# Performance work log

Measured on AMD Instinct MI355X. Metric: run time of the kernel, lower is better.

## Reference

```python
import jax, jax.numpy as jnp
from jax import lax
import numpy as np

S, B, I, H, O = 65536, 1, 2, 128, 1


def setup_inputs() -> dict:
    key = jax.random.key(0)
    k1, k2, k3, k4 = jax.random.split(key, 4)
    # xavier_normal-style scales
    s_ih = (2.0 / (4 * H + I)) ** 0.5
    s_hh = (2.0 / (4 * H + H)) ** 0.5
    s_out = (2.0 / (H + O)) ** 0.5
    return {
        "x": jax.random.normal(k1, (S, B, I), jnp.float32),
        "h0": jnp.zeros((1, B, H), jnp.float32),
        "c0": jnp.zeros((1, B, H), jnp.float32),
        "W_ih": jax.random.normal(k2, (4 * H, I), jnp.float32) * s_ih,
        "W_hh": jax.random.normal(k3, (4 * H, H), jnp.float32) * s_hh,
        "b_ih": jnp.zeros((4 * H,), jnp.float32),
        "b_hh": jnp.zeros((4 * H,), jnp.float32),
        "W_out": jax.random.normal(k4, (O, H), jnp.float32) * s_out,
        "b_out": jnp.zeros((O,), jnp.float32),
    }


def reference(x, h0, c0, W_ih, W_hh, b_ih, b_hh, W_out, b_out):
    # Precompute input-to-gate projections for all timesteps: (S, B, 4H)
    xg = jnp.einsum("sbi,gi->sbg", x, W_ih) + b_ih + b_hh

    def step(carry, xg_t):
        h, c = carry  # (B, H) each
        gates = xg_t + h @ W_hh.T  # (B, 4H); PyTorch order i,f,g,o
        i, f, g, o = jnp.split(gates, 4, axis=-1)
        i = jax.nn.sigmoid(i)
        f = jax.nn.sigmoid(f)
        g = jnp.tanh(g)
        o = jax.nn.sigmoid(o)
        c = f * c + i * g
        h = o * jnp.tanh(c)
        return (h, c), h

    (_, _), hs = lax.scan(step, (h0[0], c0[0]), xg)  # hs: (S, B, H)
    out = jnp.tanh(hs.transpose(1, 0, 2))  # (B, S, H), matches permute(1,0,2)
    out = out @ W_out.T + b_out  # (B, S, O)
    return out.reshape(out.shape[0] * out.shape[1], -1)  # (B*S, O)
```

## Files before the change

kernel.cpp:

```cpp
#include <hip/hip_runtime.h>

#define S_LEN 65536
#define HDIM 128

typedef _Float16 half2_t __attribute__((ext_vector_type(2)));
typedef _Float16 half8_t __attribute__((ext_vector_type(8)));
typedef float f32x4 __attribute__((ext_vector_type(4)));

__device__ __forceinline__ float sigm(float x) {
    return 1.0f / (1.0f + __expf(-x));
}
__device__ __forceinline__ float tanh_fast(float x) {
    return 2.0f / (1.0f + __expf(-2.0f * x)) - 1.0f;
}
__device__ __forceinline__ float dot2(half2_t a, half2_t b, float c) {
#if __has_builtin(__builtin_amdgcn_fdot2)
    return __builtin_amdgcn_fdot2(a, b, c, false);
#else
    return fmaf((float)a.x, (float)b.x, fmaf((float)a.y, (float)b.y, c));
#endif
}

__global__ __launch_bounds__(512)
__attribute__((amdgpu_waves_per_eu(2, 2)))
void lstm_seq_mfma(const float* __restrict__ x,
                   const float* __restrict__ h0,
                   const float* __restrict__ c0,
                   const float* __restrict__ W_ih,
                   const float* __restrict__ W_hh,
                   const float* __restrict__ b_ih,
                   const float* __restrict__ b_hh,
                   _Float16* __restrict__ h_hist)
{
    __shared__ __align__(16) _Float16 h_sh16[HDIM];
    __shared__ __align__(16) float gates_sh[4 * HDIM];

    const int tid  = threadIdx.x;
    const int lane = tid & 63;
    const int w    = tid >> 6;
    const int m    = lane & 15;
    const int quad = lane >> 4;

#define LOAD_AF(i, q) \
    half8_t af_##i##_##q; { \
        const float* s_ = W_hh + (size_t)(w * 64 + 16 * (i) + m) * HDIM \
                               + 32 * (q) + 8 * quad; \
        af_##i##_##q = (half8_t){ \
            (_Float16)s_[0], (_Float16)s_[1], (_Float16)s_[2], (_Float16)s_[3], \
            (_Float16)s_[4], (_Float16)s_[5], (_Float16)s_[6], (_Float16)s_[7] }; \
        asm volatile("" : "+v"(af_##i##_##q)); }
    LOAD_AF(0, 0) LOAD_AF(0, 1) LOAD_AF(0, 2) LOAD_AF(0, 3)
    LOAD_AF(1, 0) LOAD_AF(1, 1) LOAD_AF(1, 2) LOAD_AF(1, 3)
    LOAD_AF(2, 0) LOAD_AF(2, 1) LOAD_AF(2, 2) LOAD_AF(2, 3)
    LOAD_AF(3, 0) LOAD_AF(3, 1) LOAD_AF(3, 2) LOAD_AF(3, 3)
#undef LOAD_AF

    float wi0x = 0.f, wi0y = 0.f, bs0 = 0.f;
    float wi1x = 0.f, wi1y = 0.f, bs1 = 0.f;
    float wi2x = 0.f, wi2y = 0.f, bs2 = 0.f;
    float wi3x = 0.f, wi3y = 0.f, bs3 = 0.f;
    float c = 0.0f;
    if (tid < HDIM) {
        wi0x = W_ih[2 * tid];            wi0y = W_ih[2 * tid + 1];
        wi1x = W_ih[2 * (tid + 128)];    wi1y = W_ih[2 * (tid + 128) + 1];
        wi2x = W_ih[2 * (tid + 256)];    wi2y = W_ih[2 * (tid + 256) + 1];
        wi3x = W_ih[2 * (tid + 384)];    wi3y = W_ih[2 * (tid + 384) + 1];
        bs0 = b_ih[tid]       + b_hh[tid];
        bs1 = b_ih[tid + 128] + b_hh[tid + 128];
        bs2 = b_ih[tid + 256] + b_hh[tid + 256];
        bs3 = b_ih[tid + 384] + b_hh[tid + 384];
        c = c0[tid];
        h_sh16[tid] = (_Float16)h0[tid];
    }
    __syncthreads();

    const float2* xp = (const float2*)x;
    float2 xcur = {0.f, 0.f}, xnext = {0.f, 0.f};
    if (tid < HDIM) xcur = xp[0];

    half8_t bf0 = (half8_t){0,0,0,0,0,0,0,0};
    half8_t bf1 = bf0, bf2 = bf0, bf3 = bf0;

    #pragma unroll 1
    for (int t = 0; t < S_LEN; ++t) {
        if (m == 0) {
            const half8_t* hb = (const half8_t*)h_sh16;
            bf0 = hb[quad];
            bf1 = hb[4 + quad];
            bf2 = hb[8 + quad];
            bf3 = hb[12 + quad];
        }
        f32x4 acc0 = {0.f, 0.f, 0.f, 0.f};
        f32x4 acc1 = {0.f, 0.f, 0.f, 0.f};
        f32x4 acc2 = {0.f, 0.f, 0.f, 0.f};
        f32x4 acc3 = {0.f, 0.f, 0.f, 0.f};
#define MFMA_TILE(i) \
        acc##i = __builtin_amdgcn_mfma_f32_16x16x32_f16(af_##i##_0, bf0, acc##i, 0, 0, 0); \
        acc##i = __builtin_amdgcn_mfma_f32_16x16x32_f16(af_##i##_1, bf1, acc##i, 0, 0, 0); \
        acc##i = __builtin_amdgcn_mfma_f32_16x16x32_f16(af_##i##_2, bf2, acc##i, 0, 0, 0); \
        acc##i = __builtin_amdgcn_mfma_f32_16x16x32_f16(af_##i##_3, bf3, acc##i, 0, 0, 0);
        MFMA_TILE(0) MFMA_TILE(1) MFMA_TILE(2) MFMA_TILE(3)
#undef MFMA_TILE
        if (m == 0) {
            f32x4* gp = (f32x4*)gates_sh + w * 16 + quad;
            gp[0]  = acc0;
            gp[4]  = acc1;
            gp[8]  = acc2;
            gp[12] = acc3;
        }

        if (tid < HDIM) {
            const int tn = (t + 1 < S_LEN) ? (t + 1) : (S_LEN - 1);
            xnext = xp[tn];
        }
        __syncthreads();

        if (tid < HDIM) {
            float gi = sigm(gates_sh[tid]
                            + fmaf(wi0x, xcur.x, fmaf(wi0y, xcur.y, bs0)));
            float gf = sigm(gates_sh[tid + 128]
                            + fmaf(wi1x, xcur.x, fmaf(wi1y, xcur.y, bs1)));
            float gg = tanh_fast(gates_sh[tid + 256]
                            + fmaf(wi2x, xcur.x, fmaf(wi2y, xcur.y, bs2)));
            float go = sigm(gates_sh[tid + 384]
                            + fmaf(wi3x, xcur.x, fmaf(wi3y, xcur.y, bs3)));
            c = fmaf(gf, c, gi * gg);
            float h = go * tanh_fast(c);
            _Float16 hf = (_Float16)h;
            h_sh16[tid] = hf;
            h_hist[t * HDIM + tid] = hf;
            xcur = xnext;
        }
        __syncthreads();
    }
}

__global__ __launch_bounds__(256)
void out_proj(const _Float16* __restrict__ h_hist,
              const float* __restrict__ W_out,
              const float* __restrict__ b_out,
              float* __restrict__ out)
{
    const int lane  = threadIdx.x & 63;
    const int gwave = (blockIdx.x * 256 + threadIdx.x) >> 6;
    const int nwave = (gridDim.x * 256) >> 6;

    const float wo0 = W_out[2 * lane + 0];
    const float wo1 = W_out[2 * lane + 1];
    const float bout = b_out[0];

    for (int t = gwave; t < S_LEN; t += nwave) {
        half2_t hv = ((const half2_t*)(h_hist + t * HDIM))[lane];
        float p = tanh_fast((float)hv.x) * wo0 + tanh_fast((float)hv.y) * wo1;
        #pragma unroll
        for (int off = 32; off > 0; off >>= 1)
            p += __shfl_xor(p, off, 64);
        if (lane == 0) out[t] = p + bout;
    }
}

#define H_HI_OFF 144
__global__ __launch_bounds__(1024)
__attribute__((amdgpu_waves_per_eu(4, 4)))
void lstm_seq_full(const float* __restrict__ x,
                   const float* __restrict__ h0,
                   const float* __restrict__ c0,
                   const float* __restrict__ W_ih,
                   const float* __restrict__ W_hh,
                   const float* __restrict__ b_ih,
                   const float* __restrict__ b_hh,
                   const float* __restrict__ W_out,
                   const float* __restrict__ b_out,
                   float* __restrict__ out)
{
    __shared__ __align__(16) unsigned char h_raw[2 * H_HI_OFF];
    __shared__ float gates_part[2 * 512];
    __shared__ float red_sh[2];

    const int tid  = threadIdx.x;
    const int j    = tid >> 1;
    const int half = tid & 1;

    const float2* wr2 = (const float2*)(W_hh + j * HDIM + half * 64);
#define WDEF(i) half2_t W##i; { float2 t = wr2[i]; \
        W##i.x = (_Float16)t.x; W##i.y = (_Float16)t.y; } \
        asm volatile("" : "+v"(W##i));
    WDEF(0)  WDEF(1)  WDEF(2)  WDEF(3)  WDEF(4)  WDEF(5)  WDEF(6)  WDEF(7)
    WDEF(8)  WDEF(9)  WDEF(10) WDEF(11) WDEF(12) WDEF(13) WDEF(14) WDEF(15)
    WDEF(16) WDEF(17) WDEF(18) WDEF(19) WDEF(20) WDEF(21) WDEF(22) WDEF(23)
    WDEF(24) WDEF(25) WDEF(26) WDEF(27) WDEF(28) WDEF(29) WDEF(30) WDEF(31)
#undef WDEF

    float wih0 = 0.0f, wih1 = 0.0f, bias = 0.0f;
    if (half == 0) {
        wih0 = W_ih[2 * j + 0];
        wih1 = W_ih[2 * j + 1];
        bias = b_ih[j] + b_hh[j];
    }

    float c = 0.0f, wout = 0.0f;
    _Float16* hw = (_Float16*)(h_raw + ((tid < 64) ? 2 * tid
                                                   : H_HI_OFF + 2 * (tid - 64)));
    if (tid < HDIM) {
        c = c0[tid];
        wout = W_out[tid];
        *hw = (_Float16)h0[tid];
    }
    const float bout = b_out[0];
    __syncthreads();

    const float2* xp = (const float2*)x;
    float2 xcur = xp[0];
    const half8_t* hp = (const half8_t*)(h_raw + half * H_HI_OFF);

    #pragma unroll 1
    for (int t = 0; t < S_LEN; ++t) {
        const int tn = (t + 1 < S_LEN) ? (t + 1) : (S_LEN - 1);
        float2 xnext = xp[tn];

        float a0 = fmaf(wih0, xcur.x, fmaf(wih1, xcur.y, bias));
        float a1 = 0.0f, a2 = 0.0f, a3 = 0.0f;

#define CHUNK(cc, w0_, w1_, w2_, w3_) {                         \
        half8_t hv = hp[cc];                                    \
        half2_t p0 = { hv[0], hv[1] };                          \
        half2_t p1 = { hv[2], hv[3] };                          \
        half2_t p2 = { hv[4], hv[5] };                          \
        half2_t p3 = { hv[6], hv[7] };                          \
        a0 = dot2(w0_, p0, a0);                                 \
        a1 = dot2(w1_, p1, a1);                                 \
        a2 = dot2(w2_, p2, a2);                                 \
        a3 = dot2(w3_, p3, a3); }
        CHUNK(0, W0,  W1,  W2,  W3)
        CHUNK(1, W4,  W5,  W6,  W7)
        CHUNK(2, W8,  W9,  W10, W11)
        CHUNK(3, W12, W13, W14, W15)
        CHUNK(4, W16, W17, W18, W19)
        CHUNK(5, W20, W21, W22, W23)
        CHUNK(6, W24, W25, W26, W27)
        CHUNK(7, W28, W29, W30, W31)
#undef CHUNK

        gates_part[half * 512 + j] = (a0 + a1) + (a2 + a3);
        __syncthreads();

        if (tid < HDIM) {
            float gi = sigm(gates_part[tid]            + gates_part[tid + 512]);
            float gf = sigm(gates_part[tid + 128]      + gates_part[tid + 640]);
            float gg = tanh_fast(gates_part[tid + 256] + gates_part[tid + 768]);
            float go = sigm(gates_part[tid + 384]      + gates_part[tid + 896]);
            c = fmaf(gf, c, gi * gg);
            float h = go * tanh_fast(c);
            *hw = (_Float16)h;

            float p = tanh_fast(h) * wout;
            #pragma unroll
            for (int off = 32; off > 0; off >>= 1)
                p += __shfl_xor(p, off, 64);
            if ((tid & 63) == 0) red_sh[tid >> 6] = p;
        }
        __syncthreads();

        if (tid == 0) out[t] = red_sh[0] + red_sh[1] + bout;
        xcur = xnext;
    }
}

extern "C" void kernel_launch(void* const* d_in, const int* in_sizes, int n_in,
                              void* d_out, int out_size, void* d_ws, size_t ws_size,
                              hipStream_t stream) {
    const float* x     = (const float*)d_in[0];
    const float* h0    = (const float*)d_in[1];
    const float* c0    = (const float*)d_in[2];
    const float* W_ih  = (const float*)d_in[3];
    const float* W_hh  = (const float*)d_in[4];
    const float* b_ih  = (const float*)d_in[5];
    const float* b_hh  = (const float*)d_in[6];
    const float* W_out = (const float*)d_in[7];
    const float* b_out = (const float*)d_in[8];

    const size_t need = (size_t)S_LEN * HDIM * sizeof(_Float16);
    if (ws_size >= need) {
        _Float16* h_hist = (_Float16*)d_ws;
        lstm_seq_mfma<<<dim3(1), dim3(512), 0, stream>>>(
            x, h0, c0, W_ih, W_hh, b_ih, b_hh, h_hist);
        out_proj<<<dim3(1024), dim3(256), 0, stream>>>(
            h_hist, W_out, b_out, (float*)d_out);
    } else {
        lstm_seq_full<<<dim3(1), dim3(1024), 0, stream>>>(
            x, h0, c0, W_ih, W_hh, b_ih, b_hh, W_out, b_out, (float*)d_out);
    }
}
```

Baseline: 46.68 ms.

## Compute LSTM gates in MFMA lanes with double-buffered h and single barrier

Reorders W_hh rows so each wave's four MFMA tiles hold the i,f,g,o gates for the same 16 hidden units. Lanes with m<4 now apply the nonlinearities directly from their accumulator registers, which removes the gates_sh round-trip through shared memory. With h double-buffered, each timestep needs one barrier instead of two, and that barrier is a raw s_barrier. x is prefetched two steps ahead and the loop is unrolled by two. In exchange, the pointwise work is spread across all eight waves, and correctness now depends on the MFMA output layout and on the hand-placed waitcnt before the barrier.

```diff
diff --git a/kernel.cpp b/kernel.cpp
--- a/kernel.cpp
+++ b/kernel.cpp
@@ -20,6 +20,12 @@
     return fmaf((float)a.x, (float)b.x, fmaf((float)a.y, (float)b.y, c));
 #endif
 }
+
+#define WG_BARRIER() do {                                         \
+    asm volatile("s_waitcnt lgkmcnt(0)" ::: "memory");            \
+    __builtin_amdgcn_s_barrier();                                 \
+    asm volatile("" ::: "memory");                                \
+} while (0)
 
 __global__ __launch_bounds__(512)
 __attribute__((amdgpu_waves_per_eu(2, 2)))
@@ -32,8 +38,7 @@
                    const float* __restrict__ b_hh,
                    _Float16* __restrict__ h_hist)
 {
-    __shared__ __align__(16) _Float16 h_sh16[HDIM];
-    __shared__ __align__(16) float gates_sh[4 * HDIM];
+    __shared__ __align__(16) _Float16 h_buf[2][HDIM];
 
     const int tid  = threadIdx.x;
     const int lane = tid & 63;
@@ -41,98 +46,100 @@
     const int m    = lane & 15;
     const int quad = lane >> 4;
 
-#define LOAD_AF(i, q) \
-    half8_t af_##i##_##q; { \
-        const float* s_ = W_hh + (size_t)(w * 64 + 16 * (i) + m) * HDIM \
-                               + 32 * (q) + 8 * quad; \
-        af_##i##_##q = (half8_t){ \
+#define LOAD_AF(i, cc) \
+    half8_t af_##i##_##cc; { \
+        const float* s_ = W_hh + (size_t)((i) * 128 + w * 16 + m) * HDIM \
+                               + 32 * (cc) + 8 * quad; \
+        af_##i##_##cc = (half8_t){ \
             (_Float16)s_[0], (_Float16)s_[1], (_Float16)s_[2], (_Float16)s_[3], \
             (_Float16)s_[4], (_Float16)s_[5], (_Float16)s_[6], (_Float16)s_[7] }; \
-        asm volatile("" : "+v"(af_##i##_##q)); }
+        asm volatile("" : "+v"(af_##i##_##cc)); }
     LOAD_AF(0, 0) LOAD_AF(0, 1) LOAD_AF(0, 2) LOAD_AF(0, 3)
     LOAD_AF(1, 0) LOAD_AF(1, 1) LOAD_AF(1, 2) LOAD_AF(1, 3)
     LOAD_AF(2, 0) LOAD_AF(2, 1) LOAD_AF(2, 2) LOAD_AF(2, 3)
     LOAD_AF(3, 0) LOAD_AF(3, 1) LOAD_AF(3, 2) LOAD_AF(3, 3)
 #undef LOAD_AF
 
-    float wi0x = 0.f, wi0y = 0.f, bs0 = 0.f;
-    float wi1x = 0.f, wi1y = 0.f, bs1 = 0.f;
-    float wi2x = 0.f, wi2y = 0.f, bs2 = 0.f;
-    float wi3x = 0.f, wi3y = 0.f, bs3 = 0.f;
+    const bool worker = (m < 4);
+    const int  hidx   = w * 16 + quad * 4 + (m & 3);
+    float wi00 = 0.f, wi01 = 0.f, bs0 = 0.f;
+    float wi10 = 0.f, wi11 = 0.f, bs1 = 0.f;
+    float wi20 = 0.f, wi21 = 0.f, bs2 = 0.f;
+    float wi30 = 0.f, wi31 = 0.f, bs3 = 0.f;
     float c = 0.0f;
-    if (tid < HDIM) {
-        wi0x = W_ih[2 * tid];            wi0y = W_ih[2 * tid + 1];
-        wi1x = W_ih[2 * (tid + 128)];    wi1y = W_ih[2 * (tid + 128) + 1];
-        wi2x = W_ih[2 * (tid + 256)];    wi2y = W_ih[2 * (tid + 256) + 1];
-        wi3x = W_ih[2 * (tid + 384)];    wi3y = W_ih[2 * (tid + 384) + 1];
-        bs0 = b_ih[tid]       + b_hh[tid];
-        bs1 = b_ih[tid + 128] + b_hh[tid + 128];
-        bs2 = b_ih[tid + 256] + b_hh[tid + 256];
-        bs3 = b_ih[tid + 384] + b_hh[tid + 384];
-        c = c0[tid];
-        h_sh16[tid] = (_Float16)h0[tid];
-    }
+    if (worker) {
+        const int r0 = hidx;
+        const int r1 = hidx + 128;
+        const int r2 = hidx + 256;
+        const int r3 = hidx + 384;
+        wi00 = W_ih[2 * r0]; wi01 = W_ih[2 * r0 + 1]; bs0 = b_ih[r0] + b_hh[r0];
+        wi10 = W_ih[2 * r1]; wi11 = W_ih[2 * r1 + 1]; bs1 = b_ih[r1] + b_hh[r1];
+        wi20 = W_ih[2 * r2]; wi21 = W_ih[2 * r2 + 1]; bs2 = b_ih[r2] + b_hh[r2];
+        wi30 = W_ih[2 * r3]; wi31 = W_ih[2 * r3 + 1]; bs3 = b_ih[r3] + b_hh[r3];
+        c = c0[hidx];
+    }
+    if (tid < HDIM) h_buf[0][tid] = (_Float16)h0[tid];
     __syncthreads();
 
     const float2* xp = (const float2*)x;
-    float2 xcur = {0.f, 0.f}, xnext = {0.f, 0.f};
-    if (tid < HDIM) xcur = xp[0];
-
-    half8_t bf0 = (half8_t){0,0,0,0,0,0,0,0};
-    half8_t bf1 = bf0, bf2 = bf0, bf3 = bf0;
+    float2 xcur = xp[0];
+    float2 xn1  = xp[1];
+
+    const bool selod = (m & 1) != 0;
+    const bool selhi = (m & 2) != 0;
+
+#define MFMA_T(i) \
+    acc##i = __builtin_amdgcn_mfma_f32_16x16x32_f16(af_##i##_0, bf0, acc##i, 0, 0, 0); \
+    acc##i = __builtin_amdgcn_mfma_f32_16x16x32_f16(af_##i##_1, bf1, acc##i, 0, 0, 0); \
+    acc##i = __builtin_amdgcn_mfma_f32_16x16x32_f16(af_##i##_2, bf2, acc##i, 0, 0, 0); \
+    acc##i = __builtin_amdgcn_mfma_f32_16x16x32_f16(af_##i##_3, bf3, acc##i, 0, 0, 0);
+
+#define STEP(T, RB, WB) { \
+     \
+    const half8_t* hb_ = (const half8_t*)(RB); \
+    half8_t bf0 = hb_[quad]; \
+    half8_t bf1 = hb_[4 + quad]; \
+    half8_t bf2 = hb_[8 + quad]; \
+    half8_t bf3 = hb_[12 + quad]; \
+    f32x4 acc0 = {0.f, 0.f, 0.f, 0.f}; \
+    f32x4 acc1 = acc0, acc2 = acc0, acc3 = acc0; \
+    MFMA_T(0) MFMA_T(1) MFMA_T(2) MFMA_T(3) \
+    int tn_ = (T) + 2; if (tn_ >= S_LEN) tn_ = S_LEN - 1; \
+    float2 xnew_ = xp[tn_]; \
+    const float xg0 = fmaf(wi00, xcur.x, fmaf(wi01, xcur.y, bs0)); \
+    const float xg1 = fmaf(wi10, xcur.x, fmaf(wi11, xcur.y, bs1)); \
+    const float xg2 = fmaf(wi20, xcur.x, fmaf(wi21, xcur.y, bs2)); \
+    const float xg3 = fmaf(wi30, xcur.x, fmaf(wi31, xcur.y, bs3)); \
+    if (worker) { \
+        float sa_, sb_; \
+        sa_ = selod ? acc0[1] : acc0[0]; sb_ = selod ? acc0[3] : acc0[2]; \
+        const float g0 = (selhi ? sb_ : sa_) + xg0; \
+        sa_ = selod ? acc1[1] : acc1[0]; sb_ = selod ? acc1[3] : acc1[2]; \
+        const float g1 = (selhi ? sb_ : sa_) + xg1; \
+        sa_ = selod ? acc2[1] : acc2[0]; sb_ = selod ? acc2[3] : acc2[2]; \
+        const float g2 = (selhi ? sb_ : sa_) + xg2; \
+        sa_ = selod ? acc3[1] : acc3[0]; sb_ = selod ? acc3[3] : acc3[2]; \
+        const float g3 = (selhi ? sb_ : sa_) + xg3; \
+        const float gi = sigm(g0); \
+        const float gf = sigm(g1); \
+        const float gg = tanh_fast(g2); \
+        const float go = sigm(g3); \
+        c = fmaf(gf, c, gi * gg); \
+        const float hv_ = go * tanh_fast(c); \
+        const _Float16 hf_ = (_Float16)hv_; \
+        (WB)[hidx] = hf_;                        \
+        h_hist[(size_t)(T) * HDIM + hidx] = hf_;  \
+    } \
+    xcur = xn1; xn1 = xnew_; \
+    WG_BARRIER(); }
 
     #pragma unroll 1
-    for (int t = 0; t < S_LEN; ++t) {
-        if (m == 0) {
-            const half8_t* hb = (const half8_t*)h_sh16;
-            bf0 = hb[quad];
-            bf1 = hb[4 + quad];
-            bf2 = hb[8 + quad];
-            bf3 = hb[12 + quad];
-        }
-        f32x4 acc0 = {0.f, 0.f, 0.f, 0.f};
-        f32x4 acc1 = {0.f, 0.f, 0.f, 0.f};
-        f32x4 acc2 = {0.f, 0.f, 0.f, 0.f};
-        f32x4 acc3 = {0.f, 0.f, 0.f, 0.f};
-#define MFMA_TILE(i) \
-        acc##i = __builtin_amdgcn_mfma_f32_16x16x32_f16(af_##i##_0, bf0, acc##i, 0, 0, 0); \
-        acc##i = __builtin_amdgcn_mfma_f32_16x16x32_f16(af_##i##_1, bf1, acc##i, 0, 0, 0); \
-        acc##i = __builtin_amdgcn_mfma_f32_16x16x32_f16(af_##i##_2, bf2, acc##i, 0, 0, 0); \
-        acc##i = __builtin_amdgcn_mfma_f32_16x16x32_f16(af_##i##_3, bf3, acc##i, 0, 0, 0);
-        MFMA_TILE(0) MFMA_TILE(1) MFMA_TILE(2) MFMA_TILE(3)
-#undef MFMA_TILE
-        if (m == 0) {
-            f32x4* gp = (f32x4*)gates_sh + w * 16 + quad;
-            gp[0]  = acc0;
-            gp[4]  = acc1;
-            gp[8]  = acc2;
-            gp[12] = acc3;
-        }
-
-        if (tid < HDIM) {
-            const int tn = (t + 1 < S_LEN) ? (t + 1) : (S_LEN - 1);
-            xnext = xp[tn];
-        }
-        __syncthreads();
-
-        if (tid < HDIM) {
-            float gi = sigm(gates_sh[tid]
-                            + fmaf(wi0x, xcur.x, fmaf(wi0y, xcur.y, bs0)));
-            float gf = sigm(gates_sh[tid + 128]
-                            + fmaf(wi1x, xcur.x, fmaf(wi1y, xcur.y, bs1)));
-            float gg = tanh_fast(gates_sh[tid + 256]
-                            + fmaf(wi2x, xcur.x, fmaf(wi2y, xcur.y, bs2)));
-            float go = sigm(gates_sh[tid + 384]
-                            + fmaf(wi3x, xcur.x, fmaf(wi3y, xcur.y, bs3)));
-            c = fmaf(gf, c, gi * gg);
-            float h = go * tanh_fast(c);
-            _Float16 hf = (_Float16)h;
-            h_sh16[tid] = hf;
-            h_hist[t * HDIM + tid] = hf;
-            xcur = xnext;
-        }
-        __syncthreads();
-    }
+    for (int t = 0; t < S_LEN; t += 2) {
+        STEP(t,     h_buf[0], h_buf[1])
+        STEP(t + 1, h_buf[1], h_buf[0])
+    }
+#undef STEP
+#undef MFMA_T
 }
 
 __global__ __launch_bounds__(256)
```

Result: faster. 40.53 ms (-13.2%).
